# Performance work log

Measured on AMD Instinct MI355X. Metric: run time of the kernel, lower is better.

The kernel has to match this reference:

```python
import jax, jax.numpy as jnp
import numpy as np

N = 10000
E = 320000
NODE_IN, EDGE_IN, HID, LAT = 128, 64, 128, 64


def _linear_params(key, fan_in, fan_out):
    k1, k2 = jax.random.split(key)
    bound = 1.0 / np.sqrt(fan_in)
    W = jax.random.uniform(k1, (fan_in, fan_out), jnp.float32, -bound, bound)
    b = jax.random.uniform(k2, (fan_out,), jnp.float32, -bound, bound)
    return W, b


def setup_inputs() -> dict:
    key = jax.random.key(0)
    ks = jax.random.split(key, 12)
    node_features = jax.random.normal(ks[0], (N, NODE_IN), jnp.float32)
    edge_features = jax.random.normal(ks[1], (E, EDGE_IN), jnp.float32)
    src = jax.random.randint(ks[2], (E,), 0, N, jnp.int32)
    dst = jax.random.randint(ks[3], (E,), 0, N, jnp.int32)
    Wn1, bn1 = _linear_params(ks[4], NODE_IN, HID)
    We1, be1 = _linear_params(ks[5], EDGE_IN, HID)
    Wm1, bm1 = _linear_params(ks[6], HID, HID)
    Wn2, bn2 = _linear_params(ks[7], HID, LAT)
    We2, be2 = _linear_params(ks[8], EDGE_IN, LAT)
    Wm2, bm2 = _linear_params(ks[9], LAT, LAT)
    return dict(node_features=node_features, edge_features=edge_features,
                src=src, dst=dst,
                Wn1=Wn1, bn1=bn1, We1=We1, be1=be1, Wm1=Wm1, bm1=bm1,
                Wn2=Wn2, bn2=bn2, We2=We2, be2=be2, Wm2=Wm2, bm2=bm2)


def _edge_gnn_layer(x, ef, src, dst, Wn, bn, We, be, Wm, bm):
    h = x @ Wn + bn                       # [N, out]
    e = ef @ We + be                      # [E, out]
    msg = (h[src] + e) @ Wm + bm          # gather + u_add_e + msg_fc, [E, out]
    agg = jax.ops.segment_sum(msg, dst, num_segments=N)   # scatter sum [N, out]
    deg = jax.ops.segment_sum(jnp.ones((msg.shape[0],), msg.dtype), dst,
                              num_segments=N)
    return agg / jnp.maximum(deg, 1.0)[:, None]            # mean (0 for deg=0)


def reference(node_features, edge_features, src, dst,
              Wn1, bn1, We1, be1, Wm1, bm1,
              Wn2, bn2, We2, be2, Wm2, bm2):
    h1 = jax.nn.relu(_edge_gnn_layer(node_features, edge_features, src, dst,
                                     Wn1, bn1, We1, be1, Wm1, bm1))
    z = _edge_gnn_layer(h1, edge_features, src, dst,
                        Wn2, bn2, We2, be2, Wm2, bm2)      # [N, LAT]
    adj_pred = jax.nn.sigmoid(z @ z.T)                      # [N, N]
    return z, adj_pred
```

## Files before the change

### kernel.cpp

```cpp
#include <hip/hip_runtime.h>
#include <hip/hip_bf16.h>

#define NN 10000
#define NE 320000
#define F_NODE 128
#define F_EDGE 64
#define HID 128
#define LAT 64

using bf16 = __hip_bfloat16;
typedef float f32x4 __attribute__((ext_vector_type(4)));

static __device__ __forceinline__ float ldf(const void* p, long i, int isbf) {
    if (isbf) return __bfloat162float(((const bf16*)p)[i]);
    return ((const float*)p)[i];
}

__global__ void k_detect(const void* nf, const void* ef,
                         const void* w0, const void* w1, const void* w2, const void* w3,
                         const void* w4, const void* w5, const void* w6, const void* w7,
                         const void* w8, const void* w9, const void* w10, const void* w11,
                         const int* srcp, const int* dstp, int* __restrict__ flags) {
    const void* ps[14] = {nf, ef, w0, w1, w2, w3, w4, w5, w6, w7, w8, w9, w10, w11};
    const int lens[14] = {NN * F_NODE, NE * F_EDGE,
                          16384, 128, 8192, 128, 16384, 128,
                          8192, 64, 4096, 64, 4096, 64};
    __shared__ int cntr;
    if (threadIdx.x == 0) cntr = 0;
    __syncthreads();
    int b = blockIdx.x;
    if (b < 14) {
        const unsigned short* raw = (const unsigned short*)ps[b];
        int S = lens[b] / 2; if (S > 2048) S = 2048;
        int c = 0;
        for (int i = threadIdx.x; i < S; i += 256) {
            unsigned short u = raw[2 * i];
            int e = (u >> 7) & 0xFF;
            if (e < 90 || e > 160) c++;
        }
        atomicAdd(&cntr, c);
        __syncthreads();
        if (threadIdx.x == 0) flags[b] = (10 * cntr > 3 * S) ? 0 : 1;
    } else {
        const int* raw = (b == 14) ? srcp : dstp;
        int S = 2048;
        int c = 0;
        for (int i = threadIdx.x; i < S; i += 256) {
            if (raw[2 * i + 1] == 0) c++;
        }
        atomicAdd(&cntr, c);
        __syncthreads();
        if (threadIdx.x == 0) flags[b] = (2 * cntr > S) ? 1 : 0;
    }
}

__global__ void k_convert_w(const void* w0, const void* w1, const void* w2, const void* w3,
                            const void* w4, const void* w5, const void* w6, const void* w7,
                            const void* w8, const void* w9, const void* w10, const void* w11,
                            const int* __restrict__ flags, float* __restrict__ wf) {
    const int WLEN[12] = {16384, 128, 8192, 128, 16384, 128, 8192, 64, 4096, 64, 4096, 64};
    const int WOFF[12] = {0, 16384, 16512, 24704, 24832, 41216, 41344, 49536, 49600, 53696, 53760, 57856};
    const void* ps[12] = {w0, w1, w2, w3, w4, w5, w6, w7, w8, w9, w10, w11};
    int t = blockIdx.x >> 6;
    int i = (blockIdx.x & 63) * 256 + threadIdx.x;
    if (i < WLEN[t]) wf[WOFF[t] + i] = ldf(ps[t], i, flags[2 + t]);
}


__global__ void k_count(const int* __restrict__ dstp, const int* __restrict__ flags,
                        int* __restrict__ cnt) {
    int e = blockIdx.x * 256 + threadIdx.x;
    int w = flags[15];
    if (e < NE) atomicAdd(&cnt[dstp[(long)e << w]], 1);
}

__global__ void k_scan(const int* __restrict__ cnt, int* __restrict__ row_start) {
    __shared__ int buf[1024];
    __shared__ int carry;
    if (threadIdx.x == 0) carry = 0;
    __syncthreads();
    for (int base = 0; base < NN; base += 1024) {
        int i = base + threadIdx.x;
        int v = (i < NN) ? cnt[i] : 0;
        buf[threadIdx.x] = v;
        __syncthreads();
        for (int off = 1; off < 1024; off <<= 1) {
            int t = (threadIdx.x >= off) ? buf[threadIdx.x - off] : 0;
            __syncthreads();
            buf[threadIdx.x] += t;
            __syncthreads();
        }
        int excl = carry + buf[threadIdx.x] - v;
        if (i < NN) row_start[i] = excl;
        __syncthreads();
        if (threadIdx.x == 1023) carry += buf[1023];
        __syncthreads();
    }
    if (threadIdx.x == 0) row_start[NN] = carry;
}

__global__ void k_fill(const int* __restrict__ srcp, const int* __restrict__ dstp,
                       const int* __restrict__ flags,
                       const int* __restrict__ row_start, int* __restrict__ fill,
                       int2* __restrict__ epack) {
    int e = blockIdx.x * 256 + threadIdx.x;
    int ws_ = flags[14], wd = flags[15];
    if (e < NE) {
        int d = dstp[(long)e << wd];
        int s = srcp[(long)e << ws_];
        int pos = row_start[d] + atomicAdd(&fill[d], 1);
        epack[pos] = make_int2(e, s);
    }
}

__global__ void k_layer1(const void* __restrict__ nf, const void* __restrict__ ef,
                         const int* __restrict__ flags,
                         const int* __restrict__ row_start, const int* __restrict__ cnt,
                         const int2* __restrict__ epack,
                         const float* __restrict__ Wn1, const float* __restrict__ bn1,
                         const float* __restrict__ We1, const float* __restrict__ be1,
                         const float* __restrict__ Wm1, const float* __restrict__ bm1,
                         float* __restrict__ h1, float* __restrict__ bvec) {
    int n = blockIdx.x;
    int t = threadIdx.x;
    __shared__ float a_s[F_NODE], b_s[F_EDGE], t_s[HID];

    int fn = flags[0], fe = flags[1];
    int start = row_start[n], deg = cnt[n];
    float accx = 0.f, acce = 0.f;
    for (int i = 0; i < deg; i++) {
        int2 p = epack[start + i];
        accx += ldf(nf, (long)p.y * F_NODE + t, fn);
        if (t < F_EDGE) acce += ldf(ef, (long)p.x * F_EDGE + t, fe);
    }
    float inv = (deg > 0) ? (1.f / (float)deg) : 0.f;
    a_s[t] = accx * inv;
    if (t < F_EDGE) { b_s[t] = acce * inv; bvec[n * F_EDGE + t] = acce * inv; }
    __syncthreads();

    float acc = bn1[t] + be1[t];
    for (int k = 0; k < F_NODE; k++) acc += a_s[k] * Wn1[k * HID + t];
    for (int k = 0; k < F_EDGE; k++) acc += b_s[k] * We1[k * HID + t];
    t_s[t] = acc;
    __syncthreads();

    float o = bm1[t];
    for (int k = 0; k < HID; k++) o += t_s[k] * Wm1[k * HID + t];
    if (deg == 0) o = 0.f;
    o = fmaxf(o, 0.f);
    h1[n * HID + t] = o;
}

__global__ void k_layer2(const float* __restrict__ h1, const float* __restrict__ bvec,
                         const int* __restrict__ row_start, const int* __restrict__ cnt,
                         const int2* __restrict__ epack,
                         const float* __restrict__ Wn2, const float* __restrict__ bn2,
                         const float* __restrict__ We2, const float* __restrict__ be2,
                         const float* __restrict__ Wm2, const float* __restrict__ bm2,
                         float* __restrict__ z, float* __restrict__ zout) {
    int n = blockIdx.x;
    int t = threadIdx.x;
    __shared__ float a_s[HID], b_s[F_EDGE], t_s[LAT];

    int start = row_start[n], deg = cnt[n];
    float accx = 0.f;
    for (int i = 0; i < deg; i++) {
        int2 p = epack[start + i];
        accx += h1[p.y * HID + t];
    }
    float inv = (deg > 0) ? (1.f / (float)deg) : 0.f;
    a_s[t] = accx * inv;
    if (t < F_EDGE) b_s[t] = bvec[n * F_EDGE + t];
    __syncthreads();

    if (t < LAT) {
        float acc = bn2[t] + be2[t];
        for (int k = 0; k < HID; k++) acc += a_s[k] * Wn2[k * LAT + t];
        for (int k = 0; k < F_EDGE; k++) acc += b_s[k] * We2[k * LAT + t];
        t_s[t] = acc;
    }
    __syncthreads();

    if (t < LAT) {
        float o = bm2[t];
        for (int k = 0; k < LAT; k++) o += t_s[k] * Wm2[k * LAT + t];
        if (deg == 0) o = 0.f;
        z[n * LAT + t] = o;
        zout[n * LAT + t] = o;
    }
}

__global__ __launch_bounds__(256, 2) void k_adj(const float* __restrict__ z,
                                                float* __restrict__ out) {
    __shared__ float As[128 * 64];
    __shared__ float Bs[128 * 64];
    const int t  = threadIdx.x;
    const int tx = t & 15;
    const int ty = t >> 4;
    const int r0 = blockIdx.y * 128;
    const int c0 = blockIdx.x * 128;

    float4* As4w = (float4*)As;
    float4* Bs4w = (float4*)Bs;
#pragma unroll
    for (int it = 0; it < 8; ++it) {
        int idx = it * 256 + t;
        int row = idx >> 4;
        int kq  = idx & 15;
        int sw  = (row >> 3) & 7;
        int gra = r0 + row;
        int grb = c0 + row;
        float4 va = make_float4(0.f, 0.f, 0.f, 0.f);
        float4 vb = make_float4(0.f, 0.f, 0.f, 0.f);
        if (gra < NN) va = *(const float4*)(z + (size_t)gra * LAT + kq * 4);
        if (grb < NN) vb = *(const float4*)(z + (size_t)grb * LAT + kq * 4);
        As4w[row * 16 + (kq ^ sw)] = va;
        Bs4w[row * 16 + (kq ^ sw)] = vb;
    }
    __syncthreads();

    float acc[8][8] = {};
    const float4* As4 = (const float4*)As;
    const float4* Bs4 = (const float4*)Bs;
    const int sa = ty & 7;
    const int sb = tx & 7;

    for (int kb = 0; kb < 16; ++kb) {
        float4 a4[8], b4[8];
#pragma unroll
        for (int i = 0; i < 8; ++i)
            a4[i] = As4[(ty * 8 + i) * 16 + (kb ^ sa)];
#pragma unroll
        for (int j = 0; j < 8; ++j)
            b4[j] = Bs4[(tx * 8 + j) * 16 + (kb ^ sb)];
#pragma unroll
        for (int i = 0; i < 8; ++i)
#pragma unroll
            for (int j = 0; j < 8; ++j) {
                acc[i][j] += a4[i].x * b4[j].x;
                acc[i][j] += a4[i].y * b4[j].y;
                acc[i][j] += a4[i].z * b4[j].z;
                acc[i][j] += a4[i].w * b4[j].w;
            }
    }

#pragma unroll
    for (int i = 0; i < 8; ++i) {
        int gr = r0 + ty * 8 + i;
        if (gr >= NN) continue;
#pragma unroll
        for (int jj = 0; jj < 2; ++jj) {
            int gc = c0 + tx * 8 + jj * 4;
            if (gc + 3 < NN) {
                f32x4 pk;
                pk.x = 1.f / (1.f + __expf(-acc[i][jj * 4 + 0]));
                pk.y = 1.f / (1.f + __expf(-acc[i][jj * 4 + 1]));
                pk.z = 1.f / (1.f + __expf(-acc[i][jj * 4 + 2]));
                pk.w = 1.f / (1.f + __expf(-acc[i][jj * 4 + 3]));
                __builtin_nontemporal_store(pk, (f32x4*)(out + (size_t)gr * NN + gc));
            }
        }
    }
}


extern "C" void kernel_launch(void* const* d_in, const int* in_sizes, int n_in,
                              void* d_out, int out_size, void* d_ws, size_t ws_size,
                              hipStream_t stream) {
    const void* nf  = d_in[0];
    const void* ef  = d_in[1];
    const int*  src = (const int*)d_in[2];
    const int*  dst = (const int*)d_in[3];
    const void* W[12];
    for (int i = 0; i < 12; i++) W[i] = d_in[4 + i];

    char* ws = (char*)d_ws;
    size_t off = 0;
    auto alloc = [&](size_t bytes) -> void* {
        void* p = ws + off;
        off = (off + bytes + 255) & ~(size_t)255;
        return p;
    };
    int*   flags     = (int*)alloc(16 * sizeof(int));
    float* wf        = (float*)alloc(57920 * sizeof(float));
    int*   cnt       = (int*)alloc(NN * sizeof(int));
    int*   fill      = (int*)alloc(NN * sizeof(int));
    int*   row_start = (int*)alloc((NN + 1) * sizeof(int));
    int2*  epack     = (int2*)alloc((size_t)NE * sizeof(int2));
    float* bvec      = (float*)alloc((size_t)NN * F_EDGE * sizeof(float));
    float* h1        = (float*)alloc((size_t)NN * HID * sizeof(float));
    float* zf        = (float*)alloc((size_t)NN * LAT * sizeof(float));

    hipMemsetAsync(cnt, 0, NN * sizeof(int), stream);
    hipMemsetAsync(fill, 0, NN * sizeof(int), stream);

    k_detect<<<16, 256, 0, stream>>>(nf, ef,
        W[0], W[1], W[2], W[3], W[4], W[5], W[6], W[7], W[8], W[9], W[10], W[11],
        src, dst, flags);
    k_convert_w<<<12 * 64, 256, 0, stream>>>(
        W[0], W[1], W[2], W[3], W[4], W[5], W[6], W[7], W[8], W[9], W[10], W[11],
        flags, wf);

    k_count<<<(NE + 255) / 256, 256, 0, stream>>>(dst, flags, cnt);
    k_scan<<<1, 1024, 0, stream>>>(cnt, row_start);
    k_fill<<<(NE + 255) / 256, 256, 0, stream>>>(src, dst, flags, row_start, fill, epack);

    const float* Wn1 = wf + 0,     *bn1 = wf + 16384;
    const float* We1 = wf + 16512, *be1 = wf + 24704;
    const float* Wm1 = wf + 24832, *bm1 = wf + 41216;
    const float* Wn2 = wf + 41344, *bn2 = wf + 49536;
    const float* We2 = wf + 49600, *be2 = wf + 53696;
    const float* Wm2 = wf + 53760, *bm2 = wf + 57856;

    k_layer1<<<NN, 128, 0, stream>>>(nf, ef, flags, row_start, cnt, epack,
                                     Wn1, bn1, We1, be1, Wm1, bm1, h1, bvec);
    k_layer2<<<NN, 128, 0, stream>>>(h1, bvec, row_start, cnt, epack,
                                     Wn2, bn2, We2, be2, Wm2, bm2,
                                     zf, (float*)d_out);

    dim3 g((NN + 127) / 128, (NN + 127) / 128);
    k_adj<<<g, 256, 0, stream>>>(zf, (float*)d_out + (size_t)NN * LAT);
}
```

Measured before the change: 886.2 us.

## Batch four nodes per block in GNN layers, exploit adjacency symmetry, warp-shuffle scan

The layer kernels now handle four destination nodes per block. Each weight element loaded from global memory is reused across those nodes, with float4 shared-memory reads of the activations. The adjacency kernel computes only upper-triangle tiles and writes each tile plus its transpose, halving the z·zᵀ and sigmoid work. The transposed stores are column-strided and less coalesced. The single-block prefix scan is replaced by a per-thread serial chunk plus a wavefront shuffle scan, removing the many barrier-separated passes.

```diff
diff --git a/kernel.cpp b/kernel.cpp
--- a/kernel.cpp
+++ b/kernel.cpp
@@ -7,6 +7,7 @@
 #define F_EDGE 64
 #define HID 128
 #define LAT 64
+#define NPB 4
 
 using bf16 = __hip_bfloat16;
 typedef float f32x4 __attribute__((ext_vector_type(4)));
@@ -75,28 +76,38 @@
 }
 
 __global__ void k_scan(const int* __restrict__ cnt, int* __restrict__ row_start) {
-    __shared__ int buf[1024];
-    __shared__ int carry;
-    if (threadIdx.x == 0) carry = 0;
-    __syncthreads();
-    for (int base = 0; base < NN; base += 1024) {
-        int i = base + threadIdx.x;
-        int v = (i < NN) ? cnt[i] : 0;
-        buf[threadIdx.x] = v;
-        __syncthreads();
-        for (int off = 1; off < 1024; off <<= 1) {
-            int t = (threadIdx.x >= off) ? buf[threadIdx.x - off] : 0;
-            __syncthreads();
-            buf[threadIdx.x] += t;
-            __syncthreads();
-        }
-        int excl = carry + buf[threadIdx.x] - v;
-        if (i < NN) row_start[i] = excl;
-        __syncthreads();
-        if (threadIdx.x == 1023) carry += buf[1023];
-        __syncthreads();
-    }
-    if (threadIdx.x == 0) row_start[NN] = carry;
+    __shared__ int wsum[16];
+    int t = threadIdx.x;
+    int base = t * 10;
+    int v[10];
+    int s = 0;
+#pragma unroll
+    for (int i = 0; i < 10; i++) {
+        v[i] = (base + i < NN) ? cnt[base + i] : 0;
+        s += v[i];
+    }
+    int lane = t & 63;
+    int x = s;
+#pragma unroll
+    for (int off = 1; off < 64; off <<= 1) {
+        int y = __shfl_up(x, off, 64);
+        if (lane >= off) x += y;
+    }
+    if (lane == 63) wsum[t >> 6] = x;
+    __syncthreads();
+    if (t == 0) {
+        int c = 0;
+#pragma unroll
+        for (int i = 0; i < 16; i++) { int tmp = wsum[i]; wsum[i] = c; c += tmp; }
+        row_start[NN] = c;
+    }
+    __syncthreads();
+    int excl = wsum[t >> 6] + x - s;
+#pragma unroll
+    for (int i = 0; i < 10; i++) {
+        if (base + i < NN) row_start[base + i] = excl;
+        excl += v[i];
+    }
 }
 
 __global__ void k_fill(const int* __restrict__ srcp, const int* __restrict__ dstp,
@@ -113,92 +124,218 @@
     }
 }
 
-__global__ void k_layer1(const void* __restrict__ nf, const void* __restrict__ ef,
-                         const int* __restrict__ flags,
-                         const int* __restrict__ row_start, const int* __restrict__ cnt,
-                         const int2* __restrict__ epack,
-                         const float* __restrict__ Wn1, const float* __restrict__ bn1,
-                         const float* __restrict__ We1, const float* __restrict__ be1,
-                         const float* __restrict__ Wm1, const float* __restrict__ bm1,
-                         float* __restrict__ h1, float* __restrict__ bvec) {
-    int n = blockIdx.x;
+__global__ __launch_bounds__(128) void k_layer1(
+        const void* __restrict__ nf, const void* __restrict__ ef,
+        const int* __restrict__ flags,
+        const int* __restrict__ row_start, const int* __restrict__ cnt,
+        const int2* __restrict__ epack,
+        const float* __restrict__ Wn1, const float* __restrict__ bn1,
+        const float* __restrict__ We1, const float* __restrict__ be1,
+        const float* __restrict__ Wm1, const float* __restrict__ bm1,
+        float* __restrict__ h1, float* __restrict__ bvec) {
+    int n0 = blockIdx.x * NPB;
     int t = threadIdx.x;
-    __shared__ float a_s[F_NODE], b_s[F_EDGE], t_s[HID];
+    __shared__ __align__(16) float a_s[NPB][F_NODE];
+    __shared__ __align__(16) float b_s[NPB][F_EDGE];
+    __shared__ __align__(16) float t_s[NPB][HID];
 
     int fn = flags[0], fe = flags[1];
-    int start = row_start[n], deg = cnt[n];
-    float accx = 0.f, acce = 0.f;
-    for (int i = 0; i < deg; i++) {
-        int2 p = epack[start + i];
-        accx += ldf(nf, (long)p.y * F_NODE + t, fn);
-        if (t < F_EDGE) acce += ldf(ef, (long)p.x * F_EDGE + t, fe);
-    }
-    float inv = (deg > 0) ? (1.f / (float)deg) : 0.f;
-    a_s[t] = accx * inv;
-    if (t < F_EDGE) { b_s[t] = acce * inv; bvec[n * F_EDGE + t] = acce * inv; }
-    __syncthreads();
-
-    float acc = bn1[t] + be1[t];
-    for (int k = 0; k < F_NODE; k++) acc += a_s[k] * Wn1[k * HID + t];
-    for (int k = 0; k < F_EDGE; k++) acc += b_s[k] * We1[k * HID + t];
-    t_s[t] = acc;
-    __syncthreads();
-
-    float o = bm1[t];
-    for (int k = 0; k < HID; k++) o += t_s[k] * Wm1[k * HID + t];
-    if (deg == 0) o = 0.f;
-    o = fmaxf(o, 0.f);
-    h1[n * HID + t] = o;
-}
-
-__global__ void k_layer2(const float* __restrict__ h1, const float* __restrict__ bvec,
-                         const int* __restrict__ row_start, const int* __restrict__ cnt,
-                         const int2* __restrict__ epack,
-                         const float* __restrict__ Wn2, const float* __restrict__ bn2,
-                         const float* __restrict__ We2, const float* __restrict__ be2,
-                         const float* __restrict__ Wm2, const float* __restrict__ bm2,
-                         float* __restrict__ z, float* __restrict__ zout) {
-    int n = blockIdx.x;
+    int start[NPB], deg[NPB];
+    int md = 0;
+#pragma unroll
+    for (int l = 0; l < NPB; l++) {
+        start[l] = row_start[n0 + l];
+        deg[l]   = cnt[n0 + l];
+        md = max(md, deg[l]);
+    }
+    float accx[NPB] = {}, acce[NPB] = {};
+    for (int i = 0; i < md; i++) {
+#pragma unroll
+        for (int l = 0; l < NPB; l++) {
+            if (i < deg[l]) {
+                int2 p = epack[start[l] + i];
+                accx[l] += ldf(nf, (long)p.y * F_NODE + t, fn);
+                if (t < F_EDGE) acce[l] += ldf(ef, (long)p.x * F_EDGE + t, fe);
+            }
+        }
+    }
+#pragma unroll
+    for (int l = 0; l < NPB; l++) {
+        float inv = (deg[l] > 0) ? (1.f / (float)deg[l]) : 0.f;
+        a_s[l][t] = accx[l] * inv;
+        if (t < F_EDGE) {
+            float b = acce[l] * inv;
+            b_s[l][t] = b;
+            bvec[(n0 + l) * F_EDGE + t] = b;
+        }
+    }
+    __syncthreads();
+
+    float o[NPB];
+    {
+        float bb = bn1[t] + be1[t];
+#pragma unroll
+        for (int l = 0; l < NPB; l++) o[l] = bb;
+    }
+    for (int k = 0; k < F_NODE; k += 4) {
+        float w0 = Wn1[(k + 0) * HID + t];
+        float w1 = Wn1[(k + 1) * HID + t];
+        float w2 = Wn1[(k + 2) * HID + t];
+        float w3 = Wn1[(k + 3) * HID + t];
+#pragma unroll
+        for (int l = 0; l < NPB; l++) {
+            float4 a = *(const float4*)&a_s[l][k];
+            o[l] += a.x * w0 + a.y * w1 + a.z * w2 + a.w * w3;
+        }
+    }
+    for (int k = 0; k < F_EDGE; k += 4) {
+        float w0 = We1[(k + 0) * HID + t];
+        float w1 = We1[(k + 1) * HID + t];
+        float w2 = We1[(k + 2) * HID + t];
+        float w3 = We1[(k + 3) * HID + t];
+#pragma unroll
+        for (int l = 0; l < NPB; l++) {
+            float4 a = *(const float4*)&b_s[l][k];
+            o[l] += a.x * w0 + a.y * w1 + a.z * w2 + a.w * w3;
+        }
+    }
+#pragma unroll
+    for (int l = 0; l < NPB; l++) t_s[l][t] = o[l];
+    __syncthreads();
+
+    float p[NPB];
+    {
+        float bb = bm1[t];
+#pragma unroll
+        for (int l = 0; l < NPB; l++) p[l] = bb;
+    }
+    for (int k = 0; k < HID; k += 4) {
+        float w0 = Wm1[(k + 0) * HID + t];
+        float w1 = Wm1[(k + 1) * HID + t];
+        float w2 = Wm1[(k + 2) * HID + t];
+        float w3 = Wm1[(k + 3) * HID + t];
+#pragma unroll
+        for (int l = 0; l < NPB; l++) {
+            float4 a = *(const float4*)&t_s[l][k];
+            p[l] += a.x * w0 + a.y * w1 + a.z * w2 + a.w * w3;
+        }
+    }
+#pragma unroll
+    for (int l = 0; l < NPB; l++) {
+        float v = (deg[l] == 0) ? 0.f : p[l];
+        h1[(n0 + l) * HID + t] = fmaxf(v, 0.f);
+    }
+}
+
+__global__ __launch_bounds__(128) void k_layer2(
+        const float* __restrict__ h1, const float* __restrict__ bvec,
+        const int* __restrict__ row_start, const int* __restrict__ cnt,
+        const int2* __restrict__ epack,
+        const float* __restrict__ Wn2, const float* __restrict__ bn2,
+        const float* __restrict__ We2, const float* __restrict__ be2,
+        const float* __restrict__ Wm2, const float* __restrict__ bm2,
+        float* __restrict__ z, float* __restrict__ zout) {
+    int n0 = blockIdx.x * NPB;
     int t = threadIdx.x;
-    __shared__ float a_s[HID], b_s[F_EDGE], t_s[LAT];
-
-    int start = row_start[n], deg = cnt[n];
-    float accx = 0.f;
-    for (int i = 0; i < deg; i++) {
-        int2 p = epack[start + i];
-        accx += h1[p.y * HID + t];
-    }
-    float inv = (deg > 0) ? (1.f / (float)deg) : 0.f;
-    a_s[t] = accx * inv;
-    if (t < F_EDGE) b_s[t] = bvec[n * F_EDGE + t];
-    __syncthreads();
-
-    if (t < LAT) {
-        float acc = bn2[t] + be2[t];
-        for (int k = 0; k < HID; k++) acc += a_s[k] * Wn2[k * LAT + t];
-        for (int k = 0; k < F_EDGE; k++) acc += b_s[k] * We2[k * LAT + t];
-        t_s[t] = acc;
-    }
-    __syncthreads();
-
-    if (t < LAT) {
-        float o = bm2[t];
-        for (int k = 0; k < LAT; k++) o += t_s[k] * Wm2[k * LAT + t];
-        if (deg == 0) o = 0.f;
-        z[n * LAT + t] = o;
-        zout[n * LAT + t] = o;
-    }
+    __shared__ __align__(16) float a_s[NPB][HID];
+    __shared__ __align__(16) float b_s[NPB][F_EDGE];
+    __shared__ __align__(16) float t_s[NPB][LAT];
+
+    int start[NPB], deg[NPB];
+    int md = 0;
+#pragma unroll
+    for (int l = 0; l < NPB; l++) {
+        start[l] = row_start[n0 + l];
+        deg[l]   = cnt[n0 + l];
+        md = max(md, deg[l]);
+    }
+    float accx[NPB] = {};
+    for (int i = 0; i < md; i++) {
+#pragma unroll
+        for (int l = 0; l < NPB; l++) {
+            if (i < deg[l]) {
+                int2 p = epack[start[l] + i];
+                accx[l] += h1[p.y * HID + t];
+            }
+        }
+    }
+#pragma unroll
+    for (int l = 0; l < NPB; l++) {
+        float inv = (deg[l] > 0) ? (1.f / (float)deg[l]) : 0.f;
+        a_s[l][t] = accx[l] * inv;
+        if (t < F_EDGE) b_s[l][t] = bvec[(n0 + l) * F_EDGE + t];
+    }
+    __syncthreads();
+
+    const int col = t & 63;
+    const int g   = t >> 6;
+    const int l0 = 2 * g, l1 = 2 * g + 1;
+
+    float o0, o1;
+    {
+        float bb = bn2[col] + be2[col];
+        o0 = bb; o1 = bb;
+    }
+    for (int k = 0; k < HID; k += 4) {
+        float w0 = Wn2[(k + 0) * LAT + col];
+        float w1 = Wn2[(k + 1) * LAT + col];
+        float w2 = Wn2[(k + 2) * LAT + col];
+        float w3 = Wn2[(k + 3) * LAT + col];
+        float4 a0 = *(const float4*)&a_s[l0][k];
+        float4 a1 = *(const float4*)&a_s[l1][k];
+        o0 += a0.x * w0 + a0.y * w1 + a0.z * w2 + a0.w * w3;
+        o1 += a1.x * w0 + a1.y * w1 + a1.z * w2 + a1.w * w3;
+    }
+    for (int k = 0; k < F_EDGE; k += 4) {
+        float w0 = We2[(k + 0) * LAT + col];
+        float w1 = We2[(k + 1) * LAT + col];
+        float w2 = We2[(k + 2) * LAT + col];
+        float w3 = We2[(k + 3) * LAT + col];
+        float4 a0 = *(const float4*)&b_s[l0][k];
+        float4 a1 = *(const float4*)&b_s[l1][k];
+        o0 += a0.x * w0 + a0.y * w1 + a0.z * w2 + a0.w * w3;
+        o1 += a1.x * w0 + a1.y * w1 + a1.z * w2 + a1.w * w3;
+    }
+    t_s[l0][col] = o0;
+    t_s[l1][col] = o1;
+    __syncthreads();
+
+    float p0, p1;
+    {
+        float bb = bm2[col];
+        p0 = bb; p1 = bb;
+    }
+    for (int k = 0; k < LAT; k += 4) {
+        float w0 = Wm2[(k + 0) * LAT + col];
+        float w1 = Wm2[(k + 1) * LAT + col];
+        float w2 = Wm2[(k + 2) * LAT + col];
+        float w3 = Wm2[(k + 3) * LAT + col];
+        float4 a0 = *(const float4*)&t_s[l0][k];
+        float4 a1 = *(const float4*)&t_s[l1][k];
+        p0 += a0.x * w0 + a0.y * w1 + a0.z * w2 + a0.w * w3;
+        p1 += a1.x * w0 + a1.y * w1 + a1.z * w2 + a1.w * w3;
+    }
+    if (deg[l0] == 0) p0 = 0.f;
+    if (deg[l1] == 0) p1 = 0.f;
+    z[(n0 + l0) * LAT + col] = p0;
+    z[(n0 + l1) * LAT + col] = p1;
+    zout[(n0 + l0) * LAT + col] = p0;
+    zout[(n0 + l1) * LAT + col] = p1;
 }
 
 __global__ __launch_bounds__(256, 2) void k_adj(const float* __restrict__ z,
                                                 float* __restrict__ out) {
+    const int bi = blockIdx.y;
+    const int bj = blockIdx.x;
+    if (bi > bj) return;
+
     __shared__ float As[128 * 64];
     __shared__ float Bs[128 * 64];
     const int t  = threadIdx.x;
     const int tx = t & 15;
     const int ty = t >> 4;
-    const int r0 = blockIdx.y * 128;
-    const int c0 = blockIdx.x * 128;
+    const int r0 = bi * 128;
+    const int c0 = bj * 128;
 
     float4* As4w = (float4*)As;
     float4* Bs4w = (float4*)Bs;
@@ -245,6 +382,12 @@
     }
 
 #pragma unroll
+    for (int i = 0; i < 8; ++i)
+#pragma unroll
+        for (int j = 0; j < 8; ++j)
+            acc[i][j] = 1.f / (1.f + __expf(-acc[i][j]));
+
+#pragma unroll
     for (int i = 0; i < 8; ++i) {
         int gr = r0 + ty * 8 + i;
         if (gr >= NN) continue;
@@ -252,12 +395,26 @@
         for (int jj = 0; jj < 2; ++jj) {
             int gc = c0 + tx * 8 + jj * 4;
             if (gc + 3 < NN) {
-                f32x4 pk;
-                pk.x = 1.f / (1.f + __expf(-acc[i][jj * 4 + 0]));
-                pk.y = 1.f / (1.f + __expf(-acc[i][jj * 4 + 1]));
-                pk.z = 1.f / (1.f + __expf(-acc[i][jj * 4 + 2]));
-                pk.w = 1.f / (1.f + __expf(-acc[i][jj * 4 + 3]));
+                f32x4 pk = {acc[i][jj * 4 + 0], acc[i][jj * 4 + 1],
+                            acc[i][jj * 4 + 2], acc[i][jj * 4 + 3]};
                 __builtin_nontemporal_store(pk, (f32x4*)(out + (size_t)gr * NN + gc));
+            }
+        }
+    }
+
+    if (bi != bj) {
+#pragma unroll
+        for (int j = 0; j < 8; ++j) {
+            int gc = c0 + tx * 8 + j;
+            if (gc >= NN) continue;
+#pragma unroll
+            for (int ii = 0; ii < 2; ++ii) {
+                int gr = r0 + ty * 8 + ii * 4;
+                if (gr + 3 < NN) {
+                    f32x4 pk = {acc[ii * 4 + 0][j], acc[ii * 4 + 1][j],
+                                acc[ii * 4 + 2][j], acc[ii * 4 + 3][j]};
+                    __builtin_nontemporal_store(pk, (f32x4*)(out + (size_t)gc * NN + gr));
+                }
             }
         }
     }
@@ -312,11 +469,11 @@
     const float* We2 = wf + 49600, *be2 = wf + 53696;
     const float* Wm2 = wf + 53760, *bm2 = wf + 57856;
 
-    k_layer1<<<NN, 128, 0, stream>>>(nf, ef, flags, row_start, cnt, epack,
-                                     Wn1, bn1, We1, be1, Wm1, bm1, h1, bvec);
-    k_layer2<<<NN, 128, 0, stream>>>(h1, bvec, row_start, cnt, epack,
-                                     Wn2, bn2, We2, be2, Wm2, bm2,
-                                     zf, (float*)d_out);
+    k_layer1<<<NN / NPB, 128, 0, stream>>>(nf, ef, flags, row_start, cnt, epack,
+                                           Wn1, bn1, We1, be1, Wm1, bm1, h1, bvec);
+    k_layer2<<<NN / NPB, 128, 0, stream>>>(h1, bvec, row_start, cnt, epack,
+                                           Wn2, bn2, We2, be2, Wm2, bm2,
+                                           zf, (float*)d_out);
 
     dim3 g((NN + 127) / 128, (NN + 127) / 128);
     k_adj<<<g, 256, 0, stream>>>(zf, (float*)d_out + (size_t)NN * LAT);
```

Result: no change. 884.9 us (-0.1%).

## Process four nodes per block with wave-per-node gathers and faster scan

Applied to the files above, without the earlier changes.

Restructures both GNN layer kernels so each 256-thread block handles four destination nodes, one wavefront per node. Edge indices are staged in LDS, and feature rows are gathered as float2 with 4-way unrolling, using templated bf16/fp32 paths. The dense projections then reuse each weight load across two nodes per thread. The single-block scan is replaced with a per-thread serial prefix plus wave shuffle scan. This cuts per-node launch and weight-reload overhead, at the cost of more register and LDS pressure and an assumption that NN divides by NPB.

```diff
diff --git a/kernel.cpp b/kernel.cpp
--- a/kernel.cpp
+++ b/kernel.cpp
@@ -7,6 +7,7 @@
 #define F_EDGE 64
 #define HID 128
 #define LAT 64
+#define NPB 4
 
 using bf16 = __hip_bfloat16;
 typedef float f32x4 __attribute__((ext_vector_type(4)));
@@ -14,6 +15,20 @@
 static __device__ __forceinline__ float ldf(const void* p, long i, int isbf) {
     if (isbf) return __bfloat162float(((const bf16*)p)[i]);
     return ((const float*)p)[i];
+}
+
+static __device__ __forceinline__ float b2f(unsigned short u) {
+    return __uint_as_float(((unsigned int)u) << 16);
+}
+
+template<int BF>
+static __device__ __forceinline__ float2 ld2v(const void* p, int row, int C2, int lane) {
+    long idx = (long)row * C2 + lane;
+    if (BF) {
+        ushort2 v = ((const ushort2*)p)[idx];
+        return make_float2(b2f(v.x), b2f(v.y));
+    }
+    return ((const float2*)p)[idx];
 }
 
 __global__ void k_detect(const void* nf, const void* ef,
@@ -75,28 +90,38 @@
 }
 
 __global__ void k_scan(const int* __restrict__ cnt, int* __restrict__ row_start) {
-    __shared__ int buf[1024];
-    __shared__ int carry;
-    if (threadIdx.x == 0) carry = 0;
-    __syncthreads();
-    for (int base = 0; base < NN; base += 1024) {
-        int i = base + threadIdx.x;
-        int v = (i < NN) ? cnt[i] : 0;
-        buf[threadIdx.x] = v;
-        __syncthreads();
-        for (int off = 1; off < 1024; off <<= 1) {
-            int t = (threadIdx.x >= off) ? buf[threadIdx.x - off] : 0;
-            __syncthreads();
-            buf[threadIdx.x] += t;
-            __syncthreads();
-        }
-        int excl = carry + buf[threadIdx.x] - v;
-        if (i < NN) row_start[i] = excl;
-        __syncthreads();
-        if (threadIdx.x == 1023) carry += buf[1023];
-        __syncthreads();
-    }
-    if (threadIdx.x == 0) row_start[NN] = carry;
+    __shared__ int wsum[16];
+    int t = threadIdx.x;
+    int base = t * 10;
+    int v[10];
+    int s = 0;
+#pragma unroll
+    for (int i = 0; i < 10; i++) {
+        v[i] = (base + i < NN) ? cnt[base + i] : 0;
+        s += v[i];
+    }
+    int lane = t & 63;
+    int x = s;
+#pragma unroll
+    for (int off = 1; off < 64; off <<= 1) {
+        int y = __shfl_up(x, off, 64);
+        if (lane >= off) x += y;
+    }
+    if (lane == 63) wsum[t >> 6] = x;
+    __syncthreads();
+    if (t == 0) {
+        int c = 0;
+#pragma unroll
+        for (int i = 0; i < 16; i++) { int tmp = wsum[i]; wsum[i] = c; c += tmp; }
+        row_start[NN] = c;
+    }
+    __syncthreads();
+    int excl = wsum[t >> 6] + x - s;
+#pragma unroll
+    for (int i = 0; i < 10; i++) {
+        if (base + i < NN) row_start[base + i] = excl;
+        excl += v[i];
+    }
 }
 
 __global__ void k_fill(const int* __restrict__ srcp, const int* __restrict__ dstp,
@@ -113,81 +138,206 @@
     }
 }
 
-__global__ void k_layer1(const void* __restrict__ nf, const void* __restrict__ ef,
-                         const int* __restrict__ flags,
-                         const int* __restrict__ row_start, const int* __restrict__ cnt,
-                         const int2* __restrict__ epack,
-                         const float* __restrict__ Wn1, const float* __restrict__ bn1,
-                         const float* __restrict__ We1, const float* __restrict__ be1,
-                         const float* __restrict__ Wm1, const float* __restrict__ bm1,
-                         float* __restrict__ h1, float* __restrict__ bvec) {
-    int n = blockIdx.x;
+template<int FN, int FE>
+static __device__ __forceinline__ void l1_chunk(
+        const void* nf, const void* ef, const int2* e, int m, int lane,
+        float& ax0, float& ax1, float& ae0, float& ae1) {
+    int i = 0;
+    for (; i + 4 <= m; i += 4) {
+        int2 p0 = e[i], p1 = e[i + 1], p2 = e[i + 2], p3 = e[i + 3];
+        float2 x0 = ld2v<FN>(nf, p0.y, 64, lane);
+        float2 x1 = ld2v<FN>(nf, p1.y, 64, lane);
+        float2 x2 = ld2v<FN>(nf, p2.y, 64, lane);
+        float2 x3 = ld2v<FN>(nf, p3.y, 64, lane);
+        ax0 += (x0.x + x1.x) + (x2.x + x3.x);
+        ax1 += (x0.y + x1.y) + (x2.y + x3.y);
+        if (lane < 32) {
+            float2 e0 = ld2v<FE>(ef, p0.x, 32, lane);
+            float2 e1 = ld2v<FE>(ef, p1.x, 32, lane);
+            float2 e2 = ld2v<FE>(ef, p2.x, 32, lane);
+            float2 e3 = ld2v<FE>(ef, p3.x, 32, lane);
+            ae0 += (e0.x + e1.x) + (e2.x + e3.x);
+            ae1 += (e0.y + e1.y) + (e2.y + e3.y);
+        }
+    }
+    for (; i < m; ++i) {
+        int2 p = e[i];
+        float2 x = ld2v<FN>(nf, p.y, 64, lane);
+        ax0 += x.x; ax1 += x.y;
+        if (lane < 32) {
+            float2 ev = ld2v<FE>(ef, p.x, 32, lane);
+            ae0 += ev.x; ae1 += ev.y;
+        }
+    }
+}
+
+__global__ __launch_bounds__(256) void k_layer1(
+        const void* __restrict__ nf, const void* __restrict__ ef,
+        const int* __restrict__ flags,
+        const int* __restrict__ row_start, const int* __restrict__ cnt,
+        const int2* __restrict__ epack,
+        const float* __restrict__ Wn1, const float* __restrict__ bn1,
+        const float* __restrict__ We1, const float* __restrict__ be1,
+        const float* __restrict__ Wm1, const float* __restrict__ bm1,
+        float* __restrict__ h1, float* __restrict__ bvec) {
+    int n0 = blockIdx.x * NPB;
     int t = threadIdx.x;
-    __shared__ float a_s[F_NODE], b_s[F_EDGE], t_s[HID];
+    int w = t >> 6, lane = t & 63;
+    __shared__ int2 eph[NPB][128];
+    __shared__ __align__(16) float a_s[NPB][F_NODE];
+    __shared__ __align__(16) float b_s[NPB][F_EDGE];
+    __shared__ __align__(16) float t_s[NPB][HID];
+    __shared__ int deg_s[NPB];
 
     int fn = flags[0], fe = flags[1];
+    int n = n0 + w;
     int start = row_start[n], deg = cnt[n];
-    float accx = 0.f, acce = 0.f;
-    for (int i = 0; i < deg; i++) {
-        int2 p = epack[start + i];
-        accx += ldf(nf, (long)p.y * F_NODE + t, fn);
-        if (t < F_EDGE) acce += ldf(ef, (long)p.x * F_EDGE + t, fe);
+    if (lane == 0) deg_s[w] = deg;
+
+    float ax0 = 0.f, ax1 = 0.f, ae0 = 0.f, ae1 = 0.f;
+    for (int base = 0; base < deg; base += 128) {
+        int m = min(128, deg - base);
+        if (lane < m)      eph[w][lane]      = epack[start + base + lane];
+        if (64 + lane < m) eph[w][64 + lane] = epack[start + base + 64 + lane];
+        if (fn) { if (fe) l1_chunk<1,1>(nf, ef, eph[w], m, lane, ax0, ax1, ae0, ae1);
+                  else    l1_chunk<1,0>(nf, ef, eph[w], m, lane, ax0, ax1, ae0, ae1); }
+        else    { if (fe) l1_chunk<0,1>(nf, ef, eph[w], m, lane, ax0, ax1, ae0, ae1);
+                  else    l1_chunk<0,0>(nf, ef, eph[w], m, lane, ax0, ax1, ae0, ae1); }
     }
     float inv = (deg > 0) ? (1.f / (float)deg) : 0.f;
-    a_s[t] = accx * inv;
-    if (t < F_EDGE) { b_s[t] = acce * inv; bvec[n * F_EDGE + t] = acce * inv; }
-    __syncthreads();
-
-    float acc = bn1[t] + be1[t];
-    for (int k = 0; k < F_NODE; k++) acc += a_s[k] * Wn1[k * HID + t];
-    for (int k = 0; k < F_EDGE; k++) acc += b_s[k] * We1[k * HID + t];
-    t_s[t] = acc;
-    __syncthreads();
-
-    float o = bm1[t];
-    for (int k = 0; k < HID; k++) o += t_s[k] * Wm1[k * HID + t];
-    if (deg == 0) o = 0.f;
-    o = fmaxf(o, 0.f);
-    h1[n * HID + t] = o;
-}
-
-__global__ void k_layer2(const float* __restrict__ h1, const float* __restrict__ bvec,
-                         const int* __restrict__ row_start, const int* __restrict__ cnt,
-                         const int2* __restrict__ epack,
-                         const float* __restrict__ Wn2, const float* __restrict__ bn2,
-                         const float* __restrict__ We2, const float* __restrict__ be2,
-                         const float* __restrict__ Wm2, const float* __restrict__ bm2,
-                         float* __restrict__ z, float* __restrict__ zout) {
-    int n = blockIdx.x;
+    *(float2*)&a_s[w][2 * lane] = make_float2(ax0 * inv, ax1 * inv);
+    if (lane < 32) {
+        float2 b = make_float2(ae0 * inv, ae1 * inv);
+        *(float2*)&b_s[w][2 * lane] = b;
+        *(float2*)&bvec[(long)n * F_EDGE + 2 * lane] = b;
+    }
+    __syncthreads();
+
+    const int c = t & 127, hh = t >> 7;
+    const int la = 2 * hh, lb = 2 * hh + 1;
+    float o0 = bn1[c] + be1[c];
+    float o1 = o0;
+    for (int k = 0; k < F_NODE; k += 4) {
+        float w0 = Wn1[(k + 0) * HID + c];
+        float w1 = Wn1[(k + 1) * HID + c];
+        float w2 = Wn1[(k + 2) * HID + c];
+        float w3 = Wn1[(k + 3) * HID + c];
+        float4 aA = *(const float4*)&a_s[la][k];
+        float4 aB = *(const float4*)&a_s[lb][k];
+        o0 += aA.x * w0 + aA.y * w1 + aA.z * w2 + aA.w * w3;
+        o1 += aB.x * w0 + aB.y * w1 + aB.z * w2 + aB.w * w3;
+    }
+    for (int k = 0; k < F_EDGE; k += 4) {
+        float w0 = We1[(k + 0) * HID + c];
+        float w1 = We1[(k + 1) * HID + c];
+        float w2 = We1[(k + 2) * HID + c];
+        float w3 = We1[(k + 3) * HID + c];
+        float4 aA = *(const float4*)&b_s[la][k];
+        float4 aB = *(const float4*)&b_s[lb][k];
+        o0 += aA.x * w0 + aA.y * w1 + aA.z * w2 + aA.w * w3;
+        o1 += aB.x * w0 + aB.y * w1 + aB.z * w2 + aB.w * w3;
+    }
+    t_s[la][c] = o0;
+    t_s[lb][c] = o1;
+    __syncthreads();
+
+    float p0 = bm1[c], p1 = p0;
+    for (int k = 0; k < HID; k += 4) {
+        float w0 = Wm1[(k + 0) * HID + c];
+        float w1 = Wm1[(k + 1) * HID + c];
+        float w2 = Wm1[(k + 2) * HID + c];
+        float w3 = Wm1[(k + 3) * HID + c];
+        float4 aA = *(const float4*)&t_s[la][k];
+        float4 aB = *(const float4*)&t_s[lb][k];
+        p0 += aA.x * w0 + aA.y * w1 + aA.z * w2 + aA.w * w3;
+        p1 += aB.x * w0 + aB.y * w1 + aB.z * w2 + aB.w * w3;
+    }
+    if (deg_s[la] == 0) p0 = 0.f;
+    if (deg_s[lb] == 0) p1 = 0.f;
+    h1[(long)(n0 + la) * HID + c] = fmaxf(p0, 0.f);
+    h1[(long)(n0 + lb) * HID + c] = fmaxf(p1, 0.f);
+}
+
+__global__ __launch_bounds__(256) void k_layer2(
+        const float* __restrict__ h1, const float* __restrict__ bvec,
+        const int* __restrict__ row_start, const int* __restrict__ cnt,
+        const int2* __restrict__ epack,
+        const float* __restrict__ Wn2, const float* __restrict__ bn2,
+        const float* __restrict__ We2, const float* __restrict__ be2,
+        const float* __restrict__ Wm2, const float* __restrict__ bm2,
+        float* __restrict__ z, float* __restrict__ zout) {
+    int n0 = blockIdx.x * NPB;
     int t = threadIdx.x;
-    __shared__ float a_s[HID], b_s[F_EDGE], t_s[LAT];
-
+    int w = t >> 6, lane = t & 63;
+    __shared__ int2 eph[NPB][128];
+    __shared__ __align__(16) float a_s[NPB][HID];
+    __shared__ __align__(16) float b_s[NPB][F_EDGE];
+    __shared__ __align__(16) float t_s[NPB][LAT];
+
+    int n = n0 + w;
     int start = row_start[n], deg = cnt[n];
-    float accx = 0.f;
-    for (int i = 0; i < deg; i++) {
-        int2 p = epack[start + i];
-        accx += h1[p.y * HID + t];
+
+    const float2* h12 = (const float2*)h1;
+    float ax0 = 0.f, ax1 = 0.f;
+    for (int base = 0; base < deg; base += 128) {
+        int m = min(128, deg - base);
+        if (lane < m)      eph[w][lane]      = epack[start + base + lane];
+        if (64 + lane < m) eph[w][64 + lane] = epack[start + base + 64 + lane];
+        int i = 0;
+        for (; i + 4 <= m; i += 4) {
+            int2 p0 = eph[w][i], p1 = eph[w][i + 1], p2 = eph[w][i + 2], p3 = eph[w][i + 3];
+            float2 x0 = h12[(long)p0.y * 64 + lane];
+            float2 x1 = h12[(long)p1.y * 64 + lane];
+            float2 x2 = h12[(long)p2.y * 64 + lane];
+            float2 x3 = h12[(long)p3.y * 64 + lane];
+            ax0 += (x0.x + x1.x) + (x2.x + x3.x);
+            ax1 += (x0.y + x1.y) + (x2.y + x3.y);
+        }
+        for (; i < m; ++i) {
+            int2 p = eph[w][i];
+            float2 x = h12[(long)p.y * 64 + lane];
+            ax0 += x.x; ax1 += x.y;
+        }
     }
     float inv = (deg > 0) ? (1.f / (float)deg) : 0.f;
-    a_s[t] = accx * inv;
-    if (t < F_EDGE) b_s[t] = bvec[n * F_EDGE + t];
-    __syncthreads();
-
-    if (t < LAT) {
-        float acc = bn2[t] + be2[t];
-        for (int k = 0; k < HID; k++) acc += a_s[k] * Wn2[k * LAT + t];
-        for (int k = 0; k < F_EDGE; k++) acc += b_s[k] * We2[k * LAT + t];
-        t_s[t] = acc;
-    }
-    __syncthreads();
-
-    if (t < LAT) {
-        float o = bm2[t];
-        for (int k = 0; k < LAT; k++) o += t_s[k] * Wm2[k * LAT + t];
-        if (deg == 0) o = 0.f;
-        z[n * LAT + t] = o;
-        zout[n * LAT + t] = o;
-    }
+    *(float2*)&a_s[w][2 * lane] = make_float2(ax0 * inv, ax1 * inv);
+    if (lane < 32)
+        *(float2*)&b_s[w][2 * lane] = ((const float2*)bvec)[(long)n * 32 + lane];
+    __syncthreads();
+
+    const int c = lane;
+    float o = bn2[c] + be2[c];
+    for (int k = 0; k < HID; k += 4) {
+        float w0 = Wn2[(k + 0) * LAT + c];
+        float w1 = Wn2[(k + 1) * LAT + c];
+        float w2 = Wn2[(k + 2) * LAT + c];
+        float w3 = Wn2[(k + 3) * LAT + c];
+        float4 a = *(const float4*)&a_s[w][k];
+        o += a.x * w0 + a.y * w1 + a.z * w2 + a.w * w3;
+    }
+    for (int k = 0; k < F_EDGE; k += 4) {
+        float w0 = We2[(k + 0) * LAT + c];
+        float w1 = We2[(k + 1) * LAT + c];
+        float w2 = We2[(k + 2) * LAT + c];
+        float w3 = We2[(k + 3) * LAT + c];
+        float4 a = *(const float4*)&b_s[w][k];
+        o += a.x * w0 + a.y * w1 + a.z * w2 + a.w * w3;
+    }
+    t_s[w][c] = o;
+    __syncthreads();
+
+    float pz = bm2[c];
+    for (int k = 0; k < LAT; k += 4) {
+        float w0 = Wm2[(k + 0) * LAT + c];
+        float w1 = Wm2[(k + 1) * LAT + c];
+        float w2 = Wm2[(k + 2) * LAT + c];
+        float w3 = Wm2[(k + 3) * LAT + c];
+        float4 a = *(const float4*)&t_s[w][k];
+        pz += a.x * w0 + a.y * w1 + a.z * w2 + a.w * w3;
+    }
+    if (deg == 0) pz = 0.f;
+    z[(long)n * LAT + c] = pz;
+    zout[(long)n * LAT + c] = pz;
 }
 
 __global__ __launch_bounds__(256, 2) void k_adj(const float* __restrict__ z,
@@ -312,11 +462,11 @@
     const float* We2 = wf + 49600, *be2 = wf + 53696;
     const float* Wm2 = wf + 53760, *bm2 = wf + 57856;
 
-    k_layer1<<<NN, 128, 0, stream>>>(nf, ef, flags, row_start, cnt, epack,
-                                     Wn1, bn1, We1, be1, Wm1, bm1, h1, bvec);
-    k_layer2<<<NN, 128, 0, stream>>>(h1, bvec, row_start, cnt, epack,
-                                     Wn2, bn2, We2, be2, Wm2, bm2,
-                                     zf, (float*)d_out);
+    k_layer1<<<NN / NPB, 256, 0, stream>>>(nf, ef, flags, row_start, cnt, epack,
+                                           Wn1, bn1, We1, be1, Wm1, bm1, h1, bvec);
+    k_layer2<<<NN / NPB, 256, 0, stream>>>(h1, bvec, row_start, cnt, epack,
+                                           Wn2, bn2, We2, be2, Wm2, bm2,
+                                           zf, (float*)d_out);
 
     dim3 g((NN + 127) / 128, (NN + 127) / 128);
     k_adj<<<g, 256, 0, stream>>>(zf, (float*)d_out + (size_t)NN * LAT);
```

Result: faster. 815.7 us (-8.0%).
